# Kernel optimization log

Hardware: AMD Instinct MI355X
Metric: run time of the kernel (lower is better)

## Reference

```python
import jax, jax.numpy as jnp
import numpy as np

INPUT_SIZE = 512
HIDDEN_SIZE = 1024
BATCH = 64
SEQ_LEN = 512


def _xavier(key, shape):
    fan_out, fan_in = shape
    limit = float(np.sqrt(6.0 / (fan_in + fan_out)))
    return jax.random.uniform(key, shape, jnp.float32, -limit, limit)


def setup_inputs() -> dict:
    key = jax.random.key(0)
    k = jax.random.split(key, 5)
    x = jax.random.normal(k[0], (BATCH, SEQ_LEN, INPUT_SIZE), jnp.float32)
    h0 = jnp.zeros((2, BATCH, HIDDEN_SIZE), jnp.float32)
    # layer 0: input_size -> hidden_size; layer 1: hidden_size -> hidden_size
    Wxh0 = _xavier(k[1], (HIDDEN_SIZE, INPUT_SIZE))
    Whh0 = _xavier(k[2], (HIDDEN_SIZE, HIDDEN_SIZE))
    b0 = jnp.zeros((HIDDEN_SIZE,), jnp.float32)
    Wxh1 = _xavier(k[3], (HIDDEN_SIZE, HIDDEN_SIZE))
    Whh1 = _xavier(k[4], (HIDDEN_SIZE, HIDDEN_SIZE))
    b1 = jnp.zeros((HIDDEN_SIZE,), jnp.float32)
    return {"x": x, "h0": h0, "Wxh0": Wxh0, "Whh0": Whh0, "b0": b0,
            "Wxh1": Wxh1, "Whh1": Whh1, "b1": b1}


def _rnn_layer(x_seq, h_init, Wxh, Whh, b):
    # Precompute the input projection for all timesteps (one big GEMM).
    # x_seq: [B, T, I] -> xproj: [B, T, H]
    xproj = jnp.einsum('bti,hi->bth', x_seq, Wxh) + b
    xproj_t = jnp.swapaxes(xproj, 0, 1)  # [T, B, H] for scan

    def step(h_prev, xp_t):
        h_t = jnp.tanh(xp_t + h_prev @ Whh.T)
        return h_t, h_t

    h_last, outs = jax.lax.scan(step, h_init, xproj_t)
    return jnp.swapaxes(outs, 0, 1), h_last  # [B, T, H], [B, H]


def reference(x, h0, Wxh0, Whh0, b0, Wxh1, Whh1, b1):
    out0, hn0 = _rnn_layer(x, h0[0], Wxh0, Whh0, b0)
    out1, hn1 = _rnn_layer(out0, h0[1], Wxh1, Whh1, b1)
    h_n = jnp.stack([hn0, hn1], axis=0)  # [num_layers, B, H]
    return out1, h_n
```

## Files before the change

kernel.cpp:

```cpp
#include <hip/hip_runtime.h>
#include <hip/hip_fp16.h>

typedef _Float16 f16;
typedef unsigned int u32;
typedef unsigned short u16;
typedef unsigned long long u64;
typedef _Float16 f16x8 __attribute__((ext_vector_type(8)));
typedef float f32x4 __attribute__((ext_vector_type(4)));

#define B_ 64
#define T_ 512
#define I_ 512
#define H_ 1024
#define HB_ (B_ * H_)
#define NWG_ 192
#define RS_ 32768
#define XS_ 65536

__device__ __forceinline__ u64 lda64(const u32* p) {
    return __hip_atomic_load((const u64*)p, __ATOMIC_RELAXED, __HIP_MEMORY_SCOPE_AGENT);
}
__device__ __forceinline__ u32 lda32(const u32* p) {
    return __hip_atomic_load(p, __ATOMIC_RELAXED, __HIP_MEMORY_SCOPE_AGENT);
}
__device__ __forceinline__ void sta32(u32* p, u32 v) {
    __hip_atomic_store(p, v, __ATOMIC_RELAXED, __HIP_MEMORY_SCOPE_AGENT);
}
__device__ __forceinline__ void sta16(u16* p, u16 v) {
    __hip_atomic_store(p, v, __ATOMIC_RELAXED, __HIP_MEMORY_SCOPE_AGENT);
}
__device__ __forceinline__ void stflag(int* p, int v) {
    __hip_atomic_store(p, v, __ATOMIC_RELAXED, __HIP_MEMORY_SCOPE_AGENT);
}

__device__ __forceinline__ void fastpoll(const int* p, int thr) {
    int f0, f1, f2, f3; int g = 0;
    asm volatile(
        "global_load_dword %[a], %[q], off sc0 sc1\n\t"
        "global_load_dword %[b], %[q], off sc0 sc1\n\t"
        "global_load_dword %[c], %[q], off sc0 sc1\n\t"
        "global_load_dword %[d], %[q], off sc0 sc1\n\t"
        "1:\n\t"
        "s_add_u32 %[g], %[g], 1\n\t"
        "s_cmp_gt_u32 %[g], 0x400000\n\t"
        "s_cbranch_scc1 2f\n\t"
        "s_waitcnt vmcnt(3)\n\t"
        "v_cmp_lt_i32 vcc, %[a], %[t]\n\t"
        "global_load_dword %[a], %[q], off sc0 sc1\n\t"
        "s_cbranch_vccz 2f\n\t"
        "s_waitcnt vmcnt(3)\n\t"
        "v_cmp_lt_i32 vcc, %[b], %[t]\n\t"
        "global_load_dword %[b], %[q], off sc0 sc1\n\t"
        "s_cbranch_vccz 2f\n\t"
        "s_waitcnt vmcnt(3)\n\t"
        "v_cmp_lt_i32 vcc, %[c], %[t]\n\t"
        "global_load_dword %[c], %[q], off sc0 sc1\n\t"
        "s_cbranch_vccz 2f\n\t"
        "s_waitcnt vmcnt(3)\n\t"
        "v_cmp_lt_i32 vcc, %[d], %[t]\n\t"
        "global_load_dword %[d], %[q], off sc0 sc1\n\t"
        "s_cbranch_vccnz 1b\n\t"
        "2:\n\t"
        "s_waitcnt vmcnt(0)\n\t"
        : [a]"=&v"(f0), [b]"=&v"(f1), [c]"=&v"(f2), [d]"=&v"(f3), [g]"+s"(g)
        : [q]"v"(p), [t]"v"(thr)
        : "vcc", "memory");
}

__global__ void cvt_f16(const float* __restrict__ s, f16* __restrict__ d, long n) {
    long i = ((long)blockIdx.x * blockDim.x + threadIdx.x) * 4;
    long stride = (long)gridDim.x * blockDim.x * 4;
    for (; i < n; i += stride) {
        float4 v = *reinterpret_cast<const float4*>(s + i);
        d[i+0] = (f16)v.x; d[i+1] = (f16)v.y; d[i+2] = (f16)v.z; d[i+3] = (f16)v.w;
    }
}

__global__ void init_rings(const float* __restrict__ h0,
                           u16* __restrict__ ring0, u16* __restrict__ ring1) {
    int i = blockIdx.x * blockDim.x + threadIdx.x;
    int b = i >> 10, n = i & 1023;
    int mi = b >> 4, rl = b & 15;
    int kwin = n >> 8, krem = n & 255;
    int it = krem >> 5, k32 = krem & 31;
    int kq3 = k32 >> 3, k8 = k32 & 7;
    int idx = (((mi*4 + kwin)*8 + it)*256 + (k8>>2)*128 + kq3*32 + rl*2 + ((k8>>1)&1))*2 + (k8&1);
    ring0[3*RS_*2 + idx] = __builtin_bit_cast(u16, (f16)h0[i]);
    ring1[3*RS_*2 + idx] = __builtin_bit_cast(u16, (f16)h0[HB_ + i]);
}

__global__ __launch_bounds__(256) void gemm_xproj(
    const f16* __restrict__ A, const f16* __restrict__ W,
    const float* __restrict__ bias, f16* __restrict__ out)
{
    const int wave = threadIdx.x >> 6, lane = threadIdx.x & 63;
    const int m0 = blockIdx.x << 4;
    const int r = lane & 15, kq = lane >> 4;
    const int ngrp = (blockIdx.y << 8) + (wave << 6);
    const f16* pa = A + (long)(m0 + r) * I_ + kq * 8;
    const f16* pw = W + (long)(ngrp + r) * I_ + kq * 8;

    f32x4 acc[4] = {};
    #pragma unroll
    for (int kc = 0; kc < I_; kc += 32) {
        f16x8 af = *reinterpret_cast<const f16x8*>(pa + kc);
        #pragma unroll
        for (int t = 0; t < 4; ++t) {
            f16x8 wf = *reinterpret_cast<const f16x8*>(pw + (long)t * 16 * I_ + kc);
            acc[t] = __builtin_amdgcn_mfma_f32_16x16x32_f16(af, wf, acc[t], 0, 0, 0);
        }
    }
    const int col = lane & 15, rq = lane >> 4;
    #pragma unroll
    for (int t = 0; t < 4; ++t) {
        const int n = ngrp + t * 16 + col;
        const float bv = bias[n];
        #pragma unroll
        for (int j = 0; j < 4; ++j)
            out[(long)(m0 + rq * 4 + j) * H_ + n] = (f16)(acc[t][j] + bv);
    }
}

__global__ void __launch_bounds__(256, 1) rnn_scan(
    const f16* __restrict__ Whh0, const f16* __restrict__ Wxh1, const f16* __restrict__ Whh1,
    const f16* __restrict__ xp0, const float* __restrict__ b1,
    u32* __restrict__ ring0, u32* __restrict__ ring1, u32* __restrict__ xp1,
    float* __restrict__ out, int* __restrict__ flags)
{
    extern __shared__ char smem[];
    float* part = (float*)(smem + 131072);

    const int tid = threadIdx.x;
    const int wave = tid >> 6, lane = tid & 63;
    const int wg = blockIdx.x;
    const int grp = wg >> 6, sub = wg & 63;
    const int mi = sub & 3, ct = sub >> 2;
    const int m0 = mi << 4;
    const int nbase = ct << 6;
    const int r = lane & 15, kq = lane >> 4;

    int* fAw = flags;
    int* fEw = flags + 8192;
    int* fCw = flags + 16384;
    int* fB  = flags + 24576;
    int* fD  = flags + 26624;
    const int mb4 = mi * 16;

    const f16* Wmat = (grp == 0) ? Whh0 : (grp == 1) ? Wxh1 : Whh1;

    for (int i = 0; i < 32; ++i) {
        int idx = tid + (i << 8);
        int row = idx >> 7, c = idx & 127;
        f32x4 v = *reinterpret_cast<const f32x4*>(Wmat + (long)(nbase + row) * H_ + (c << 3));
        *reinterpret_cast<f32x4*>(smem + row * 2048 + ((c ^ (row & 7)) << 4)) = v;
    }
    __syncthreads();

    const int nf = nbase + (wave << 4) + r;
    const float b1v = (grp == 1) ? b1[nf] : 0.f;

    const int kwin_s = nf >> 8, krem_s = nf & 255;
    const int it_s = krem_s >> 5, k32_s = krem_s & 31;
    const int kq3_s = k32_s >> 3, k8_s = k32_s & 7;
    const int base16 = (((mi*4 + kwin_s)*8 + it_s)*256 + (k8_s>>2)*128 + kq3_s*32 + ((k8_s>>1)&1))*2 + (k8_s&1);

    const int cBase = (mi * 4 + wave) * 2048 + (lane << 1);

    const int idx16 = lane & 15;
    const int ctp = (wave << 2) + (idx16 >> 2);
    const int wvp = idx16 & 3;
    const int myflag = ((mb4 + ct) * 4 + wave) * 32;
    const int* poll_p; int poll_d;
    if (grp == 0) {
        if (lane < 16)      { poll_p = fAw + ((mb4 + ctp) * 4 + wvp) * 32; poll_d = 0; }
        else if (lane < 32) { poll_p = fB + (mb4 + idx16) * 32;            poll_d = -3; }
        else                { poll_p = fAw + myflag;                        poll_d = -1000000; }
    } else if (grp == 1) {
        if (lane < 16)      { poll_p = fAw + ((mb4 + ctp) * 4 + wvp) * 32; poll_d = 1; }
        else if (lane == 16){ poll_p = fD + (mb4 + ct) * 32;               poll_d = -3; }
        else                { poll_p = fCw + myflag;                        poll_d = -1000000; }
    } else {
        if (lane < 16)      { poll_p = fEw + ((mb4 + ctp) * 4 + wvp) * 32; poll_d = 0; }
        else if (lane == 16){ poll_p = fCw + ((mb4 + ct) * 4 + wave) * 32; poll_d = 1; }
        else                { poll_p = fEw + myflag;                        poll_d = -1000000; }
    }

    for (int ts = 0; ts < T_; ++ts) {
        float xv[4];
        if (grp == 0) {
            #pragma unroll
            for (int j = 0; j < 4; ++j)
                xv[j] = (float)xp0[((long)(m0 + kq * 4 + j) * T_ + ts) * H_ + nf];
        } else {
            #pragma unroll
            for (int j = 0; j < 4; ++j) xv[j] = 0.f;
        }

        fastpoll(poll_p, ts + poll_d);
        __builtin_amdgcn_sched_barrier(0);

        const u32* ringA;
        if (grp == 0)      ringA = ring0 + ((ts - 1) & 3) * RS_;
        else if (grp == 1) ringA = ring0 + (ts & 3) * RS_;
        else               ringA = ring1 + ((ts - 1) & 3) * RS_;

        if (grp == 2) {
            #pragma unroll
            for (int j = 0; j < 4; ++j)
                xv[j] = __builtin_bit_cast(float,
                    lda32(xp1 + (ts & 3) * XS_ + (m0 + kq * 4 + j) * 1024 + nf));
        }

        const u32* abase = ringA + cBase;
        u64 q[8][2];
        #pragma unroll
        for (int it = 0; it < 8; ++it) {
            q[it][0] = lda64(abase + it * 256);
            q[it][1] = lda64(abase + it * 256 + 128);
        }

        f16x8 ah[8];
        #pragma unroll
        for (int it = 0; it < 8; ++it) {
            u32 w0 = (u32)q[it][0], w1 = (u32)(q[it][0] >> 32);
            u32 w2 = (u32)q[it][1], w3 = (u32)(q[it][1] >> 32);
            ah[it][0] = __builtin_bit_cast(f16, (u16)(w0 & 0xffff));
            ah[it][1] = __builtin_bit_cast(f16, (u16)(w0 >> 16));
            ah[it][2] = __builtin_bit_cast(f16, (u16)(w1 & 0xffff));
            ah[it][3] = __builtin_bit_cast(f16, (u16)(w1 >> 16));
            ah[it][4] = __builtin_bit_cast(f16, (u16)(w2 & 0xffff));
            ah[it][5] = __builtin_bit_cast(f16, (u16)(w2 >> 16));
            ah[it][6] = __builtin_bit_cast(f16, (u16)(w3 & 0xffff));
            ah[it][7] = __builtin_bit_cast(f16, (u16)(w3 >> 16));
        }
        asm volatile("s_waitcnt vmcnt(0)" ::: "memory");
        __builtin_amdgcn_sched_barrier(0);

        f32x4 acc[4] = {};
        #pragma unroll
        for (int it = 0; it < 8; ++it) {
            #pragma unroll
            for (int t = 0; t < 4; ++t) {
                f16x8 wf = *reinterpret_cast<const f16x8*>(
                    smem + (t * 16 + r) * 2048
                         + ((((wave << 5) + (it << 2) + kq) ^ (r & 7)) << 4));
                acc[t] = __builtin_amdgcn_mfma_f32_16x16x32_f16(ah[it], wf, acc[t], 0, 0, 0);
            }
        }
        #pragma unroll
        for (int t = 0; t < 4; ++t)
            *reinterpret_cast<f32x4*>(&part[((wave << 2) + t) * 256 + (lane << 2)]) = acc[t];
        __syncthreads();

        if (tid == 0) {
            if (grp == 1)      stflag(fB + (mb4 + ct) * 32, ts + 1);
            else if (grp == 2) stflag(fD + (mb4 + ct) * 32, ts + 1);
        }

        {
            f32x4 sm = *reinterpret_cast<f32x4*>(&part[wave * 256 + (lane << 2)]);
            #pragma unroll
            for (int w2 = 1; w2 < 4; ++w2)
                sm = sm + *reinterpret_cast<f32x4*>(&part[((w2 << 2) + wave) * 256 + (lane << 2)]);
            #pragma unroll
            for (int j = 0; j < 4; ++j) {
                const int b = m0 + kq * 4 + j;
                float v = sm[j];
                if (grp == 0) {
                    v = tanhf(v + xv[j]);
                    sta16((u16*)ring0 + (ts & 3) * RS_ * 2 + base16 + (kq * 4 + j) * 4,
                          __builtin_bit_cast(u16, (f16)v));
                    if (ts == T_ - 1) out[(long)B_ * T_ * H_ + (long)b * H_ + nf] = v;
                } else if (grp == 1) {
                    sta32(xp1 + (ts & 3) * XS_ + b * 1024 + nf, __builtin_bit_cast(u32, v + b1v));
                } else {
                    v = tanhf(v + xv[j]);
                    sta16((u16*)ring1 + (ts & 3) * RS_ * 2 + base16 + (kq * 4 + j) * 4,
                          __builtin_bit_cast(u16, (f16)v));
                    out[((long)b * T_ + ts) * H_ + nf] = v;
                    if (ts == T_ - 1) out[(long)B_ * T_ * H_ + HB_ + (long)b * H_ + nf] = v;
                }
            }
        }
        asm volatile("s_waitcnt vmcnt(0)" ::: "memory");
        if (lane == 0) {
            if (grp == 0)      stflag(fAw + myflag, ts + 1);
            else if (grp == 1) stflag(fCw + myflag, ts + 1);
            else               stflag(fEw + myflag, ts + 1);
        }
        __syncthreads();
    }
}

extern "C" void kernel_launch(void* const* d_in, const int* in_sizes, int n_in,
                              void* d_out, int out_size, void* d_ws, size_t ws_size,
                              hipStream_t stream) {
    const float* x    = (const float*)d_in[0];
    const float* h0   = (const float*)d_in[1];
    const float* Wxh0 = (const float*)d_in[2];
    const float* Whh0 = (const float*)d_in[3];
    const float* b0   = (const float*)d_in[4];
    const float* Wxh1 = (const float*)d_in[5];
    const float* Whh1 = (const float*)d_in[6];
    const float* b1   = (const float*)d_in[7];
    float* out = (float*)d_out;

    char* ws = (char*)d_ws;
    const long MB = 1024 * 1024;
    f16* Whh0h = (f16*)(ws + 0);
    f16* Wxh1h = (f16*)(ws + 2*MB);
    f16* Whh1h = (f16*)(ws + 4*MB);
    f16* Wxh0h = (f16*)(ws + 6*MB);
    int* flags = (int*)(ws + 7*MB);
    u32* ring0 = (u32*)(ws + 8*MB);
    u32* ring1 = (u32*)(ws + 9*MB);
    u32* xp1   = (u32*)(ws + 10*MB);
    f16* xp0   = (f16*)(ws + 16*MB);
    f16* xh    = (f16*)(ws + 80*MB);

    cvt_f16<<<512, 256, 0, stream>>>(Whh0, Whh0h, (long)H_*H_);
    cvt_f16<<<512, 256, 0, stream>>>(Wxh1, Wxh1h, (long)H_*H_);
    cvt_f16<<<512, 256, 0, stream>>>(Whh1, Whh1h, (long)H_*H_);
    cvt_f16<<<512, 256, 0, stream>>>(Wxh0, Wxh0h, (long)H_*I_);
    cvt_f16<<<4096, 256, 0, stream>>>(x, xh, (long)B_*T_*I_);
    init_rings<<<HB_/256, 256, 0, stream>>>(h0, (u16*)ring0, (u16*)ring1);
    hipMemsetAsync(flags, 0, 128*1024, stream);

    gemm_xproj<<<dim3((B_*T_)/16, H_/256), 256, 0, stream>>>(xh, Wxh0h, b0, xp0);

    hipFuncSetAttribute((const void*)rnn_scan,
                        hipFuncAttributeMaxDynamicSharedMemorySize, 147456);

    void* args[] = { (void*)&Whh0h, (void*)&Wxh1h, (void*)&Whh1h, (void*)&xp0,
                     (void*)&b1, (void*)&ring0, (void*)&ring1, (void*)&xp1,
                     (void*)&out, (void*)&flags };
    hipLaunchCooperativeKernel((void*)rnn_scan, dim3(NWG_), dim3(256), args,
                               147456, stream);
}
```

Baseline: 2.297 ms.

## Fuse f32-to-f16 conversions into consumers and shrink xp1 exchange to f16

Removes the five standalone cvt_f16 launches. The conversion of x and Wxh0 now happens inside the projection GEMM, and the conversion of the recurrent weights happens while they are staged into LDS in the scan kernel. The GEMM tile widens to 128 columns per wave, which halves the grid in N, so each A fragment is reused across eight MFMAs. The layer-1 input projection exchanged between groups is stored as f16 instead of f32, halving that traffic but adding rounding to the layer-1 input.

```diff
diff --git a/kernel.cpp b/kernel.cpp
--- a/kernel.cpp
+++ b/kernel.cpp
@@ -15,22 +15,20 @@
 #define HB_ (B_ * H_)
 #define NWG_ 192
 #define RS_ 32768
-#define XS_ 65536
+#define XS16_ 65536
 
 __device__ __forceinline__ u64 lda64(const u32* p) {
     return __hip_atomic_load((const u64*)p, __ATOMIC_RELAXED, __HIP_MEMORY_SCOPE_AGENT);
 }
-__device__ __forceinline__ u32 lda32(const u32* p) {
-    return __hip_atomic_load(p, __ATOMIC_RELAXED, __HIP_MEMORY_SCOPE_AGENT);
-}
-__device__ __forceinline__ void sta32(u32* p, u32 v) {
-    __hip_atomic_store(p, v, __ATOMIC_RELAXED, __HIP_MEMORY_SCOPE_AGENT);
-}
 __device__ __forceinline__ void sta16(u16* p, u16 v) {
     __hip_atomic_store(p, v, __ATOMIC_RELAXED, __HIP_MEMORY_SCOPE_AGENT);
 }
 __device__ __forceinline__ void stflag(int* p, int v) {
     __hip_atomic_store(p, v, __ATOMIC_RELAXED, __HIP_MEMORY_SCOPE_AGENT);
+}
+__device__ __forceinline__ float ldxf16(const u16* p) {
+    u16 v = __hip_atomic_load(p, __ATOMIC_RELAXED, __HIP_MEMORY_SCOPE_AGENT);
+    return (float)__builtin_bit_cast(f16, v);
 }
 
 __device__ __forceinline__ void fastpoll(const int* p, int thr) {
@@ -67,15 +65,6 @@
         : "vcc", "memory");
 }
 
-__global__ void cvt_f16(const float* __restrict__ s, f16* __restrict__ d, long n) {
-    long i = ((long)blockIdx.x * blockDim.x + threadIdx.x) * 4;
-    long stride = (long)gridDim.x * blockDim.x * 4;
-    for (; i < n; i += stride) {
-        float4 v = *reinterpret_cast<const float4*>(s + i);
-        d[i+0] = (f16)v.x; d[i+1] = (f16)v.y; d[i+2] = (f16)v.z; d[i+3] = (f16)v.w;
-    }
-}
-
 __global__ void init_rings(const float* __restrict__ h0,
                            u16* __restrict__ ring0, u16* __restrict__ ring1) {
     int i = blockIdx.x * blockDim.x + threadIdx.x;
@@ -90,29 +79,36 @@
 }
 
 __global__ __launch_bounds__(256) void gemm_xproj(
-    const f16* __restrict__ A, const f16* __restrict__ W,
+    const float* __restrict__ A, const float* __restrict__ W,
     const float* __restrict__ bias, f16* __restrict__ out)
 {
     const int wave = threadIdx.x >> 6, lane = threadIdx.x & 63;
     const int m0 = blockIdx.x << 4;
     const int r = lane & 15, kq = lane >> 4;
-    const int ngrp = (blockIdx.y << 8) + (wave << 6);
-    const f16* pa = A + (long)(m0 + r) * I_ + kq * 8;
-    const f16* pw = W + (long)(ngrp + r) * I_ + kq * 8;
-
-    f32x4 acc[4] = {};
+    const int ngrp = (blockIdx.y << 9) + (wave << 7);
+    const float* pa = A + (long)(m0 + r) * I_ + kq * 8;
+    const float* pw = W + (long)(ngrp + r) * I_ + kq * 8;
+
+    f32x4 acc[8] = {};
     #pragma unroll
     for (int kc = 0; kc < I_; kc += 32) {
-        f16x8 af = *reinterpret_cast<const f16x8*>(pa + kc);
-        #pragma unroll
-        for (int t = 0; t < 4; ++t) {
-            f16x8 wf = *reinterpret_cast<const f16x8*>(pw + (long)t * 16 * I_ + kc);
+        float4 a0 = *reinterpret_cast<const float4*>(pa + kc);
+        float4 a1 = *reinterpret_cast<const float4*>(pa + kc + 4);
+        f16x8 af = { (f16)a0.x, (f16)a0.y, (f16)a0.z, (f16)a0.w,
+                     (f16)a1.x, (f16)a1.y, (f16)a1.z, (f16)a1.w };
+        #pragma unroll
+        for (int t = 0; t < 8; ++t) {
+            const float* pwt = pw + (long)t * 16 * I_ + kc;
+            float4 w0 = *reinterpret_cast<const float4*>(pwt);
+            float4 w1 = *reinterpret_cast<const float4*>(pwt + 4);
+            f16x8 wf = { (f16)w0.x, (f16)w0.y, (f16)w0.z, (f16)w0.w,
+                         (f16)w1.x, (f16)w1.y, (f16)w1.z, (f16)w1.w };
             acc[t] = __builtin_amdgcn_mfma_f32_16x16x32_f16(af, wf, acc[t], 0, 0, 0);
         }
     }
     const int col = lane & 15, rq = lane >> 4;
     #pragma unroll
-    for (int t = 0; t < 4; ++t) {
+    for (int t = 0; t < 8; ++t) {
         const int n = ngrp + t * 16 + col;
         const float bv = bias[n];
         #pragma unroll
@@ -122,9 +118,9 @@
 }
 
 __global__ void __launch_bounds__(256, 1) rnn_scan(
-    const f16* __restrict__ Whh0, const f16* __restrict__ Wxh1, const f16* __restrict__ Whh1,
+    const float* __restrict__ Whh0, const float* __restrict__ Wxh1, const float* __restrict__ Whh1,
     const f16* __restrict__ xp0, const float* __restrict__ b1,
-    u32* __restrict__ ring0, u32* __restrict__ ring1, u32* __restrict__ xp1,
+    u32* __restrict__ ring0, u32* __restrict__ ring1, u16* __restrict__ xp1,
     float* __restrict__ out, int* __restrict__ flags)
 {
     extern __shared__ char smem[];
@@ -146,13 +142,17 @@
     int* fD  = flags + 26624;
     const int mb4 = mi * 16;
 
-    const f16* Wmat = (grp == 0) ? Whh0 : (grp == 1) ? Wxh1 : Whh1;
+    const float* Wmat = (grp == 0) ? Whh0 : (grp == 1) ? Wxh1 : Whh1;
 
     for (int i = 0; i < 32; ++i) {
         int idx = tid + (i << 8);
         int row = idx >> 7, c = idx & 127;
-        f32x4 v = *reinterpret_cast<const f32x4*>(Wmat + (long)(nbase + row) * H_ + (c << 3));
-        *reinterpret_cast<f32x4*>(smem + row * 2048 + ((c ^ (row & 7)) << 4)) = v;
+        const float* src = Wmat + (long)(nbase + row) * H_ + (c << 3);
+        float4 w0 = *reinterpret_cast<const float4*>(src);
+        float4 w1 = *reinterpret_cast<const float4*>(src + 4);
+        f16x8 wf = { (f16)w0.x, (f16)w0.y, (f16)w0.z, (f16)w0.w,
+                     (f16)w1.x, (f16)w1.y, (f16)w1.z, (f16)w1.w };
+        *reinterpret_cast<f16x8*>(smem + row * 2048 + ((c ^ (row & 7)) << 4)) = wf;
     }
     __syncthreads();
 
@@ -207,8 +207,7 @@
         if (grp == 2) {
             #pragma unroll
             for (int j = 0; j < 4; ++j)
-                xv[j] = __builtin_bit_cast(float,
-                    lda32(xp1 + (ts & 3) * XS_ + (m0 + kq * 4 + j) * 1024 + nf));
+                xv[j] = ldxf16(xp1 + (ts & 3) * XS16_ + (m0 + kq * 4 + j) * 1024 + nf);
         }
 
         const u32* abase = ringA + cBase;
@@ -272,7 +271,8 @@
                           __builtin_bit_cast(u16, (f16)v));
                     if (ts == T_ - 1) out[(long)B_ * T_ * H_ + (long)b * H_ + nf] = v;
                 } else if (grp == 1) {
-                    sta32(xp1 + (ts & 3) * XS_ + b * 1024 + nf, __builtin_bit_cast(u32, v + b1v));
+                    sta16(xp1 + (ts & 3) * XS16_ + b * 1024 + nf,
+                          __builtin_bit_cast(u16, (f16)(v + b1v)));
                 } else {
                     v = tanhf(v + xv[j]);
                     sta16((u16*)ring1 + (ts & 3) * RS_ * 2 + base16 + (kq * 4 + j) * 4,
@@ -307,31 +307,21 @@
 
     char* ws = (char*)d_ws;
     const long MB = 1024 * 1024;
-    f16* Whh0h = (f16*)(ws + 0);
-    f16* Wxh1h = (f16*)(ws + 2*MB);
-    f16* Whh1h = (f16*)(ws + 4*MB);
-    f16* Wxh0h = (f16*)(ws + 6*MB);
     int* flags = (int*)(ws + 7*MB);
     u32* ring0 = (u32*)(ws + 8*MB);
     u32* ring1 = (u32*)(ws + 9*MB);
-    u32* xp1   = (u32*)(ws + 10*MB);
+    u16* xp1   = (u16*)(ws + 10*MB);
     f16* xp0   = (f16*)(ws + 16*MB);
-    f16* xh    = (f16*)(ws + 80*MB);
-
-    cvt_f16<<<512, 256, 0, stream>>>(Whh0, Whh0h, (long)H_*H_);
-    cvt_f16<<<512, 256, 0, stream>>>(Wxh1, Wxh1h, (long)H_*H_);
-    cvt_f16<<<512, 256, 0, stream>>>(Whh1, Whh1h, (long)H_*H_);
-    cvt_f16<<<512, 256, 0, stream>>>(Wxh0, Wxh0h, (long)H_*I_);
-    cvt_f16<<<4096, 256, 0, stream>>>(x, xh, (long)B_*T_*I_);
+
     init_rings<<<HB_/256, 256, 0, stream>>>(h0, (u16*)ring0, (u16*)ring1);
     hipMemsetAsync(flags, 0, 128*1024, stream);
 
-    gemm_xproj<<<dim3((B_*T_)/16, H_/256), 256, 0, stream>>>(xh, Wxh0h, b0, xp0);
+    gemm_xproj<<<dim3((B_*T_)/16, H_/512), 256, 0, stream>>>(x, Wxh0, b0, xp0);
 
     hipFuncSetAttribute((const void*)rnn_scan,
                         hipFuncAttributeMaxDynamicSharedMemorySize, 147456);
 
-    void* args[] = { (void*)&Whh0h, (void*)&Wxh1h, (void*)&Whh1h, (void*)&xp0,
+    void* args[] = { (void*)&Whh0, (void*)&Wxh1, (void*)&Whh1, (void*)&xp0,
                      (void*)&b1, (void*)&ring0, (void*)&ring1, (void*)&xp1,
                      (void*)&out, (void*)&flags };
     hipLaunchCooperativeKernel((void*)rnn_scan, dim3(NWG_), dim3(256), args,
```

Result: slower. 2.750 ms (+19.7%).
